# Performance work log

Hardware: AMD Instinct MI355X
Metric: run time of the kernel (lower is better)

Reference implementation:

```python
import jax, jax.numpy as jnp
import numpy as np

DIM = 33  # hardcoded in the torch module


def setup_inputs() -> dict:
    key = jax.random.key(0)
    k1, k2, k3 = jax.random.split(key, 3)
    B, H, W = 8, 512, 512
    inp = jax.random.uniform(k1, (B, 3, H, W), dtype=jnp.float32)
    out = jax.random.uniform(k2, (B, 3, H, W), dtype=jnp.float32)
    mask = (jax.random.uniform(k3, (B, 1, H, W)) > 0.5).astype(jnp.float32)
    return {"mask": mask, "input": inp, "output": out}


def _tridistribute(mask, inp, out, dim=DIM):
    # Trilinear scatter-accumulate of `out` pixel colors into a per-image
    # 3D LUT indexed by `inp` pixel colors, masked, then count-normalized.
    B = inp.shape[0]
    binsize = 1.000001 / (dim - 1)
    x = inp / binsize                              # [B,3,H,W]
    idx = jnp.floor(x).astype(jnp.int32)           # lower bin ids, in [0, dim-2]
    frac = x - jnp.floor(x)                        # trilinear fractions
    r_id, g_id, b_id = idx[:, 0], idx[:, 1], idx[:, 2]
    rd = frac[:, 0].reshape(B, -1)                 # [B,N], N = H*W
    gd = frac[:, 1].reshape(B, -1)
    bd = frac[:, 2].reshape(B, -1)
    base = (r_id + g_id * dim + b_id * dim * dim).reshape(B, -1)  # flat corner 000
    m = (mask[:, 0] > 0).astype(inp.dtype).reshape(B, -1)
    ws, offs = [], []
    for db in (0, 1):
        for dg in (0, 1):
            for dr in (0, 1):
                w = ((rd if dr else 1 - rd) * (gd if dg else 1 - gd) * (bd if db else 1 - bd))
                ws.append(w * m)
                offs.append(dr + dg * dim + db * dim * dim)
    w_all = jnp.stack(ws, 0)                                        # [8,B,N]
    idx_all = base[None] + jnp.asarray(offs, jnp.int32)[:, None, None]  # [8,B,N]
    idx_flat = idx_all.transpose(1, 0, 2).reshape(B, -1)            # [B,8N]
    w_flat = w_all.transpose(1, 0, 2).reshape(B, -1)                # [B,8N]
    out_f = out.reshape(B, 3, -1)                                   # [B,3,N]
    vals = (w_all[:, :, None, :] * out_f[None]).transpose(1, 2, 0, 3).reshape(B, 3, -1)  # [B,3,8N]
    nbins = dim ** 3
    # scatter-add per batch element (vmap over B, then over 3 channels)
    lut = jax.vmap(lambda i, v: jax.vmap(lambda vc: jnp.zeros(nbins, inp.dtype).at[i].add(vc))(v))(idx_flat, vals)  # [B,3,nbins]
    cnt1 = jax.vmap(lambda i, w: jnp.zeros(nbins, inp.dtype).at[i].add(w))(idx_flat, w_flat)  # [B,nbins]
    cnt = jnp.broadcast_to(cnt1[:, None, :], lut.shape)             # same count for all 3 channels
    denom = jnp.where(cnt > 0, cnt, 1.0)
    lut = jnp.where(cnt > 0, lut / denom, 0.0)                      # tridistribute.divide
    shape5 = (B, 3, dim, dim, dim)
    return lut.reshape(shape5), cnt.reshape(shape5)


def reference(mask, input, output):
    lut, lut_count = _tridistribute(mask, input, output)
    return lut, lut_count, output
```

## Files before the change

### kernel.cpp

```cpp
#include <hip/hip_runtime.h>
#include <hip/hip_fp16.h>

#define DIM   33
#define NB    (DIM * DIM * DIM)
#define BATCH 8
#define HW    (512 * 512)
#define SLICE (DIM * DIM)
#define NK1   32
#define CAP1  4416
#define W1    256
#define SPAN1 1024
#define SUB2  4
#define NKEY  1024
#define CAP2  192
#define MAXC2 1120

#define G1_OFF 0
#define G2_OFF 256
#define NCNT   (G2_OFF + BATCH * NKEY)
#define A1     8448
#define S1     (BATCH * NK1 * CAP1)
#define A2     (A1 + 3 * S1)
#define S2     (BATCH * NKEY * CAP2)
#define WS_WORDS (A2 + 3 * S2)

static __device__ __forceinline__ unsigned f2h(float x) {
    return (unsigned)__half_as_ushort(__float2half(x));
}
static __device__ __forceinline__ float h2f(unsigned u) {
    return __half2float(__ushort_as_half((unsigned short)(u & 0xffffu)));
}
static __device__ __forceinline__ unsigned pack2(float a, float b) {
    return f2h(a) | (f2h(b) << 16);
}

__global__ __launch_bounds__(256) void zero_counters(int* __restrict__ ws)
{
    int i = blockIdx.x * 256 + threadIdx.x;
    if (i < NCNT) ws[i] = 0;
}

__global__ __launch_bounds__(256) void sort1(const float* __restrict__ mask,
                                             const float* __restrict__ inp,
                                             const float* __restrict__ outp,
                                             int* __restrict__ ws,
                                             float* __restrict__ outcopy)
{
    __shared__ int hist[NK1], basev[NK1], startL[NK1];
    __shared__ unsigned       stX[SPAN1];
    __shared__ unsigned       stY[SPAN1];
    __shared__ unsigned       o01[SPAN1];
    __shared__ unsigned short o2h[SPAN1];
    __shared__ unsigned short rnk[SPAN1];
    __shared__ unsigned short sidx[SPAN1];

    const int bid = blockIdx.x;
    const int w   = bid & (W1 - 1);
    const int b   = bid >> 8;

    if (threadIdx.x < NK1) hist[threadIdx.x] = 0;
    __syncthreads();

    const float binsize = 1.000001f / 32.0f;
    const size_t off = (size_t)w * SPAN1;
    const float* mk  = mask + (size_t)b * HW + off;
    const float* inR = inp  + (size_t)b * 3 * HW + off;
    const float* inG = inR + HW;
    const float* inB = inR + 2 * HW;
    const float* oR  = outp + (size_t)b * 3 * HW + off;
    const float* oG  = oR + HW;
    const float* oB  = oR + 2 * HW;
    float* cR = outcopy + (size_t)b * 3 * HW + off;
    float* cG = cR + HW;
    float* cB = cR + 2 * HW;

    const int o = threadIdx.x * 4;

    {
        float4 mv = *(const float4*)(mk + o);
        float4 rv = *(const float4*)(inR + o);
        float4 gv = *(const float4*)(inG + o);
        float4 bv = *(const float4*)(inB + o);
        float4 a0 = *(const float4*)(oR + o);
        float4 a1 = *(const float4*)(oG + o);
        float4 a2 = *(const float4*)(oB + o);

        *(float4*)(cR + o) = a0;
        *(float4*)(cG + o) = a1;
        *(float4*)(cB + o) = a2;

        float mm[4] = {mv.x, mv.y, mv.z, mv.w};
        float rr[4] = {rv.x, rv.y, rv.z, rv.w};
        float gg[4] = {gv.x, gv.y, gv.z, gv.w};
        float bb[4] = {bv.x, bv.y, bv.z, bv.w};
        float q0[4] = {a0.x, a0.y, a0.z, a0.w};
        float q1[4] = {a1.x, a1.y, a1.z, a1.w};
        float q2[4] = {a2.x, a2.y, a2.z, a2.w};
        #pragma unroll
        for (int r = 0; r < 4; ++r) {
            o01[o + r] = pack2(q0[r], q1[r]);
            o2h[o + r] = (unsigned short)f2h(q2[r]);
            unsigned sx = 0, sy = 0;
            if (mm[r] > 0.0f) {
                float xr = rr[r] / binsize;
                float xg = gg[r] / binsize;
                float xb = bb[r] / binsize;
                float fr = floorf(xr), fg = floorf(xg), fb = floorf(xb);
                int ir = (int)fr, ig = (int)fg, ib = (int)fb;
                int rd12 = (int)((xr - fr) * 4095.0f + 0.5f);
                int gd12 = (int)((xg - fg) * 4095.0f + 0.5f);
                int bd12 = (int)((xb - fb) * 4095.0f + 0.5f);
                sx = (unsigned)ir | ((unsigned)ig << 5) | ((unsigned)rd12 << 10)
                   | ((unsigned)(gd12 & 0x3FF) << 22);
                sy = (unsigned)(gd12 >> 10) | ((unsigned)bd12 << 2)
                   | ((unsigned)ib << 14) | (1u << 19);
                rnk[o + r] = (unsigned short)atomicAdd(&hist[ib], 1);
            }
            stX[o + r] = sx;
            stY[o + r] = sy;
        }
    }
    __syncthreads();

    if (threadIdx.x < NK1) {
        int c = hist[threadIdx.x];
        basev[threadIdx.x] = c ? atomicAdd(&ws[G1_OFF + b * NK1 + threadIdx.x], c) : 0;
        int v = c;
        #pragma unroll
        for (int d = 1; d < 32; d <<= 1) {
            int t = __shfl_up(v, d);
            if (threadIdx.x >= d) v += t;
        }
        startL[threadIdx.x] = v - c;
    }
    __syncthreads();

    {
        #pragma unroll
        for (int r = 0; r < 4; ++r) {
            unsigned sy = stY[o + r];
            if (sy >> 19) {
                int k = (sy >> 14) & 31;
                sidx[startL[k] + rnk[o + r]] = (unsigned short)(o + r);
            }
        }
    }
    __syncthreads();

    const int nlive = startL[NK1 - 1] + hist[NK1 - 1];
    unsigned* x1 = (unsigned*)(ws + A1);
    unsigned* y1 = x1 + S1;
    unsigned* z1 = x1 + 2 * S1;
    for (int j = threadIdx.x; j < nlive; j += 256) {
        int t = sidx[j];
        unsigned sy = stY[t];
        int k = (sy >> 14) & 31;
        int gs = basev[k] + (j - startL[k]);
        if (gs < CAP1) {
            size_t base = (size_t)(b * NK1 + k) * CAP1 + gs;
            x1[base] = stX[t];
            y1[base] = (sy & 0x3FFFu) | ((o01[t] & 0xFFFFu) << 14);
            z1[base] = (o01[t] >> 16) | ((unsigned)o2h[t] << 16);
        }
    }
}

__global__ __launch_bounds__(256) void sort2(int* __restrict__ ws)
{
    __shared__ unsigned       xL[MAXC2], yL[MAXC2], zL[MAXC2];
    __shared__ unsigned short rnkL[MAXC2], sidxL[MAXC2];
    __shared__ int hist[32], basev[32], startL[32];

    const int bid = blockIdx.x;
    const int s   = bid & (SUB2 - 1);
    const int ib  = (bid >> 2) & 31;
    const int b   = bid >> 7;

    if (threadIdx.x < 32) hist[threadIdx.x] = 0;
    __syncthreads();

    int n1 = ws[G1_OFF + b * NK1 + ib];
    if (n1 > CAP1) n1 = CAP1;
    const int beg = n1 * s / SUB2;
    const int end = n1 * (s + 1) / SUB2;
    const int cntn = end - beg;

    const unsigned* x1 = (const unsigned*)(ws + A1);
    const unsigned* y1 = x1 + S1;
    const unsigned* z1 = x1 + 2 * S1;
    const size_t base1 = (size_t)(b * NK1 + ib) * CAP1 + beg;

    for (int i = threadIdx.x; i < cntn; i += 256) {
        unsigned x = x1[base1 + i];
        xL[i] = x;
        yL[i] = y1[base1 + i];
        zL[i] = z1[base1 + i];
        rnkL[i] = (unsigned short)atomicAdd(&hist[(x >> 5) & 31], 1);
    }
    __syncthreads();

    if (threadIdx.x < 32) {
        int c = hist[threadIdx.x];
        basev[threadIdx.x] = c
            ? atomicAdd(&ws[G2_OFF + ((b << 10) | (threadIdx.x << 5) | ib)], c) : 0;
        int v = c;
        #pragma unroll
        for (int d = 1; d < 32; d <<= 1) {
            int t = __shfl_up(v, d);
            if (threadIdx.x >= d) v += t;
        }
        startL[threadIdx.x] = v - c;
    }
    __syncthreads();

    for (int i = threadIdx.x; i < cntn; i += 256) {
        int k = (xL[i] >> 5) & 31;
        sidxL[startL[k] + rnkL[i]] = (unsigned short)i;
    }
    __syncthreads();

    unsigned* x2 = (unsigned*)(ws + A2);
    unsigned* y2 = x2 + S2;
    unsigned* z2 = x2 + 2 * S2;
    for (int j = threadIdx.x; j < cntn; j += 256) {
        int t = sidxL[j];
        unsigned x = xL[t];
        int k = (x >> 5) & 31;
        int gs = basev[k] + (j - startL[k]);
        if (gs < CAP2) {
            size_t b2 = (size_t)((b << 10) | (k << 5) | ib) * CAP2 + gs;
            x2[b2] = x;
            y2[b2] = yL[t];
            z2[b2] = zL[t];
        }
    }
}

__global__ __launch_bounds__(256) void gather_pass(const int* __restrict__ ws,
                                                   float* __restrict__ lut,
                                                   float* __restrict__ cnt)
{
    __shared__ float4         vK[4][2][CAP2];
    __shared__ unsigned short sidxL[4][CAP2];
    __shared__ int            histL[4][32];
    __shared__ int            startL[4][32];
    __shared__ float          partL[4][64][4];

    const int bid   = blockIdx.x;
    const int b     = bid / SLICE;
    const int rem   = bid % SLICE;
    const int gOut  = rem / DIM;
    const int blOut = rem % DIM;

    const int wv    = threadIdx.x >> 6;
    const int lane  = threadIdx.x & 63;
    const int ghalf = (wv >> 1) & 1;
    const int bhalf = wv & 1;
    const int ig    = gOut - 1 + ghalf;
    const int ib    = blOut - 1 + bhalf;
    const bool valid = ((unsigned)ig < 32u) && ((unsigned)ib < 32u);

    if (lane < 32) histL[wv][lane] = 0;
    __syncthreads();

    const unsigned* x2 = (const unsigned*)(ws + A2);
    const unsigned* y2 = x2 + S2;
    const unsigned* z2 = x2 + 2 * S2;

    const float inv = 1.0f / 4095.0f;
    int n = 0;
    int ranks[3] = {0, 0, 0};
    int irs[3]   = {0, 0, 0};
    if (valid) {
        int key = (ig << 5) | ib;
        n = ws[G2_OFF + ((b << 10) | key)];
        if (n > CAP2) n = CAP2;
        size_t kb = (size_t)((b << 10) | key) * CAP2;
        #pragma unroll
        for (int t = 0; t < 3; ++t) {
            int i = lane + t * 64;
            if (i < n) {
                unsigned x = x2[kb + i];
                unsigned y = y2[kb + i];
                unsigned z = z2[kb + i];
                float rd = (float)((x >> 10) & 0xFFF) * inv;
                float gd = (float)(((x >> 22) & 0x3FF) | ((y & 3u) << 10)) * inv;
                float bd = (float)((y >> 2) & 0xFFF) * inv;
                float o0 = h2f(y >> 14);
                float o1 = h2f(z);
                float o2 = h2f(z >> 16);
                float wg_ = ghalf ? (1.0f - gd) : gd;
                float wb_ = bhalf ? (1.0f - bd) : bd;
                float wgb = wg_ * wb_;
                float w0 = wgb * rd;
                float w1 = wgb * (1.0f - rd);
                vK[wv][0][i] = make_float4(w0 * o0, w0 * o1, w0 * o2, w0);
                vK[wv][1][i] = make_float4(w1 * o0, w1 * o1, w1 * o2, w1);
                irs[t] = x & 31;
                ranks[t] = atomicAdd(&histL[wv][irs[t]], 1);
            }
        }
    }
    __syncthreads();

    {
        int h = (lane < 32) ? histL[wv][lane] : 0;
        int v = h;
        #pragma unroll
        for (int o = 1; o < 32; o <<= 1) {
            int t = __shfl_up(v, o, 32);
            if ((lane & 31) >= o) v += t;
        }
        if (lane < 32) startL[wv][lane] = v - h;
    }
    __syncthreads();

    if (valid) {
        #pragma unroll
        for (int t = 0; t < 3; ++t) {
            int i = lane + t * 64;
            if (i < n)
                sidxL[wv][startL[wv][irs[t]] + ranks[t]] = (unsigned short)i;
        }
    }
    __syncthreads();

    float4 acc = make_float4(0.f, 0.f, 0.f, 0.f);
    if (valid) {
        const int run = lane >> 1;
        const int kk  = lane & 1;
        int s = startL[wv][run];
        int e = s + histL[wv][run];
        for (int j = s; j < e; ++j) {
            float4 v = vK[wv][kk][sidxL[wv][j]];
            acc.x += v.x; acc.y += v.y; acc.z += v.z; acc.w += v.w;
        }
    }
    *(float4*)partL[wv][lane] = acc;
    __syncthreads();

    if (threadIdx.x < DIM * 4) {
        int r  = threadIdx.x >> 2;
        int ch = threadIdx.x & 3;
        float v = 0.f, c = 0.f;
        #pragma unroll
        for (int w2 = 0; w2 < 4; ++w2) {
            if (r < 32) {
                v += partL[w2][2 * r + 1][ch == 3 ? 3 : ch];
                c += partL[w2][2 * r + 1][3];
            }
            if (r > 0) {
                v += partL[w2][2 * r - 2][ch == 3 ? 3 : ch];
                c += partL[w2][2 * r - 2][3];
            }
        }
        int bin = r + gOut * DIM + blOut * SLICE;
        size_t ob = (size_t)b * 3 * NB;
        if (ch == 3) {
            cnt[ob + bin]          = c;
            cnt[ob + NB + bin]     = c;
            cnt[ob + 2 * NB + bin] = c;
        } else {
            lut[ob + (size_t)ch * NB + bin] = (c > 0.0f) ? v / c : 0.0f;
        }
    }
}

__global__ void tridist_scatter(const float* __restrict__ mask,
                                const float* __restrict__ inp,
                                const float* __restrict__ outp,
                                float* __restrict__ lut,
                                float* __restrict__ cnt)
{
    int i = blockIdx.x * blockDim.x + threadIdx.x;
    if (i >= BATCH * HW) return;
    int b = i / HW;
    int p = i - b * HW;

    float m = mask[(size_t)b * HW + p];
    if (!(m > 0.0f)) return;

    const float binsize = 1.000001f / 32.0f;
    size_t ibase = (size_t)b * 3 * HW + p;
    float xr = inp[ibase] / binsize;
    float xg = inp[ibase + HW] / binsize;
    float xb = inp[ibase + 2 * HW] / binsize;
    float flr = floorf(xr), flg = floorf(xg), flb = floorf(xb);
    int ir = (int)flr, ig = (int)flg, ib = (int)flb;
    float rd = xr - flr, gd = xg - flg, bd = xb - flb;
    int base = ir + ig * DIM + ib * DIM * DIM;
    float o0 = outp[ibase], o1 = outp[ibase + HW], o2 = outp[ibase + 2 * HW];
    float wr[2] = {1.0f - rd, rd};
    float wg_[2] = {1.0f - gd, gd};
    float wb[2] = {1.0f - bd, bd};
    float* lut0 = lut + (size_t)b * 3 * NB;
    float* cnt0 = cnt + (size_t)b * 3 * NB;
    #pragma unroll
    for (int db = 0; db < 2; ++db)
        #pragma unroll
        for (int dg = 0; dg < 2; ++dg)
            #pragma unroll
            for (int dr = 0; dr < 2; ++dr) {
                float wv2 = (wr[dr] * wg_[dg]) * wb[db];
                int bin = base + dr + dg * DIM + db * DIM * DIM;
                atomicAdd(cnt0 + bin, wv2);
                atomicAdd(lut0 + bin, wv2 * o0);
                atomicAdd(lut0 + NB + bin, wv2 * o1);
                atomicAdd(lut0 + 2 * NB + bin, wv2 * o2);
            }
}

__global__ void tridist_finalize(float* __restrict__ lut, float* __restrict__ cnt)
{
    int i = blockIdx.x * blockDim.x + threadIdx.x;
    if (i >= BATCH * NB) return;
    int b = i / NB;
    int j = i - b * NB;
    float c = cnt[(size_t)b * 3 * NB + j];
    bool nz = (c > 0.0f);
    #pragma unroll
    for (int ch = 0; ch < 3; ++ch) {
        size_t off = ((size_t)b * 3 + ch) * NB + j;
        float v = lut[off];
        lut[off] = nz ? (v / c) : 0.0f;
        cnt[off] = c;
    }
}

__global__ void copy_out(const float4* __restrict__ src,
                         float4* __restrict__ dst, int n4)
{
    int i = blockIdx.x * blockDim.x + threadIdx.x;
    int stride = gridDim.x * blockDim.x;
    for (; i < n4; i += stride) dst[i] = src[i];
}

extern "C" void kernel_launch(void* const* d_in, const int* in_sizes, int n_in,
                              void* d_out, int out_size, void* d_ws, size_t ws_size,
                              hipStream_t stream)
{
    const float* mask = (const float*)d_in[0];
    const float* inp  = (const float*)d_in[1];
    const float* outp = (const float*)d_in[2];

    float* out     = (float*)d_out;
    float* lut     = out;
    float* cnt     = out + (size_t)BATCH * 3 * NB;
    float* outcopy = out + (size_t)2 * BATCH * 3 * NB;

    size_t need = (size_t)WS_WORDS * sizeof(int);

    if (ws_size >= need) {
        int* ws = (int*)d_ws;
        zero_counters<<<(NCNT + 255) / 256, 256, 0, stream>>>(ws);
        sort1<<<BATCH * W1, 256, 0, stream>>>(mask, inp, outp, ws, outcopy);
        sort2<<<BATCH * NK1 * SUB2, 256, 0, stream>>>(ws);
        gather_pass<<<BATCH * SLICE, 256, 0, stream>>>(ws, lut, cnt);
    } else {
        hipMemsetAsync(out, 0, (size_t)2 * BATCH * 3 * NB * sizeof(float), stream);
        tridist_scatter<<<(BATCH * HW + 255) / 256, 256, 0, stream>>>(mask, inp, outp, lut, cnt);
        tridist_finalize<<<(BATCH * NB + 255) / 256, 256, 0, stream>>>(lut, cnt);
        int n4 = BATCH * 3 * HW / 4;
        copy_out<<<2048, 256, 0, stream>>>((const float4*)outp, (float4*)outcopy, n4);
    }
}
```

Before: 71.65 us.

## Sort second pass fully by (g,r) bins and precompute run offsets for gather

The second sort pass now uses one 1024-thread block per (batch, b-bin) and sorts entries by the combined g and r bin in a single 1024-bin histogram and block-wide scan. It writes per-key counts and per-r run offsets into a new workspace table, so the global atomics and the counter zeroing for the second level go away. The gather kernel then reads contiguous runs directly instead of rebuilding a local histogram, scan and index permutation, which removes two barriers and the shared-memory indirection. In exchange, fewer and larger sort blocks run, and the data is read from global memory twice instead of being staged in LDS.

Result: slower. 78.74 us (+9.9%).

```diff
diff --git a/kernel.cpp b/kernel.cpp
--- a/kernel.cpp
+++ b/kernel.cpp
@@ -10,19 +10,19 @@
 #define CAP1  4416
 #define W1    256
 #define SPAN1 1024
-#define SUB2  4
 #define NKEY  1024
 #define CAP2  192
-#define MAXC2 1120
 
 #define G1_OFF 0
 #define G2_OFF 256
-#define NCNT   (G2_OFF + BATCH * NKEY)
+#define NCNT   256
 #define A1     8448
 #define S1     (BATCH * NK1 * CAP1)
 #define A2     (A1 + 3 * S1)
 #define S2     (BATCH * NKEY * CAP2)
-#define WS_WORDS (A2 + 3 * S2)
+#define RT_OFF (A2 + 3 * S2)
+#define RT_U16 (BATCH * NKEY * 32)
+#define WS_WORDS (RT_OFF + RT_U16 / 2)
 
 static __device__ __forceinline__ unsigned f2h(float x) {
     return (unsigned)__half_as_ushort(__float2half(x));
@@ -165,86 +165,109 @@
     }
 }
 
-__global__ __launch_bounds__(256) void sort2(int* __restrict__ ws)
-{
-    __shared__ unsigned       xL[MAXC2], yL[MAXC2], zL[MAXC2];
-    __shared__ unsigned short rnkL[MAXC2], sidxL[MAXC2];
-    __shared__ int hist[32], basev[32], startL[32];
-
-    const int bid = blockIdx.x;
-    const int s   = bid & (SUB2 - 1);
-    const int ib  = (bid >> 2) & 31;
-    const int b   = bid >> 7;
-
-    if (threadIdx.x < 32) hist[threadIdx.x] = 0;
+__global__ __launch_bounds__(1024) void sort2(int* __restrict__ ws,
+                                              unsigned short* __restrict__ runsT)
+{
+    __shared__ int hist[1024];
+    __shared__ int startL[1024];
+    __shared__ int wsum[16];
+
+    const int ib = blockIdx.x & 31;
+    const int b  = blockIdx.x >> 5;
+    const int tid = threadIdx.x;
+
+    hist[tid] = 0;
     __syncthreads();
 
     int n1 = ws[G1_OFF + b * NK1 + ib];
     if (n1 > CAP1) n1 = CAP1;
-    const int beg = n1 * s / SUB2;
-    const int end = n1 * (s + 1) / SUB2;
-    const int cntn = end - beg;
 
     const unsigned* x1 = (const unsigned*)(ws + A1);
     const unsigned* y1 = x1 + S1;
     const unsigned* z1 = x1 + 2 * S1;
-    const size_t base1 = (size_t)(b * NK1 + ib) * CAP1 + beg;
-
-    for (int i = threadIdx.x; i < cntn; i += 256) {
-        unsigned x = x1[base1 + i];
-        xL[i] = x;
-        yL[i] = y1[base1 + i];
-        zL[i] = z1[base1 + i];
-        rnkL[i] = (unsigned short)atomicAdd(&hist[(x >> 5) & 31], 1);
-    }
-    __syncthreads();
-
-    if (threadIdx.x < 32) {
-        int c = hist[threadIdx.x];
-        basev[threadIdx.x] = c
-            ? atomicAdd(&ws[G2_OFF + ((b << 10) | (threadIdx.x << 5) | ib)], c) : 0;
-        int v = c;
-        #pragma unroll
-        for (int d = 1; d < 32; d <<= 1) {
+    const size_t base1 = (size_t)(b * NK1 + ib) * CAP1;
+
+    int rnk[5], bins[5];
+    #pragma unroll
+    for (int k = 0; k < 5; ++k) {
+        int i = tid + k * 1024;
+        bins[k] = 0; rnk[k] = 0;
+        if (i < n1) {
+            unsigned x = x1[base1 + i];
+            int bin = (((x >> 5) & 31) << 5) | (x & 31);
+            bins[k] = bin;
+            rnk[k] = atomicAdd(&hist[bin], 1);
+        }
+    }
+    __syncthreads();
+
+    int h = hist[tid];
+    {
+        int lane = tid & 63, wid = tid >> 6;
+        int v = h;
+        #pragma unroll
+        for (int d = 1; d < 64; d <<= 1) {
             int t = __shfl_up(v, d);
-            if (threadIdx.x >= d) v += t;
-        }
-        startL[threadIdx.x] = v - c;
-    }
-    __syncthreads();
-
-    for (int i = threadIdx.x; i < cntn; i += 256) {
-        int k = (xL[i] >> 5) & 31;
-        sidxL[startL[k] + rnkL[i]] = (unsigned short)i;
-    }
-    __syncthreads();
+            if (lane >= d) v += t;
+        }
+        if (lane == 63) wsum[wid] = v;
+        __syncthreads();
+        if (tid < 16) {
+            int s = wsum[tid];
+            int v2 = s;
+            #pragma unroll
+            for (int d = 1; d < 16; d <<= 1) {
+                int t = __shfl_up(v2, d);
+                if (tid >= d) v2 += t;
+            }
+            wsum[tid] = v2 - s;
+        }
+        __syncthreads();
+        startL[tid] = v - h + wsum[wid];
+    }
+    __syncthreads();
+
+    {
+        int ig = tid >> 5, ir = tid & 31;
+        int key = (b << 10) | (ig << 5) | ib;
+        int keybase = startL[ig << 5];
+        if (ir == 0) {
+            int next = (ig == 31) ? n1 : startL[(ig + 1) << 5];
+            ws[G2_OFF + key] = next - keybase;
+            runsT[(size_t)key * 32] = 0;
+        } else {
+            runsT[(size_t)key * 32 + ir] =
+                (unsigned short)(startL[(ig << 5) | ir] - keybase);
+        }
+    }
 
     unsigned* x2 = (unsigned*)(ws + A2);
     unsigned* y2 = x2 + S2;
     unsigned* z2 = x2 + 2 * S2;
-    for (int j = threadIdx.x; j < cntn; j += 256) {
-        int t = sidxL[j];
-        unsigned x = xL[t];
-        int k = (x >> 5) & 31;
-        int gs = basev[k] + (j - startL[k]);
-        if (gs < CAP2) {
-            size_t b2 = (size_t)((b << 10) | (k << 5) | ib) * CAP2 + gs;
-            x2[b2] = x;
-            y2[b2] = yL[t];
-            z2[b2] = zL[t];
+    #pragma unroll
+    for (int k = 0; k < 5; ++k) {
+        int i = tid + k * 1024;
+        if (i < n1) {
+            int bin = bins[k];
+            int rel = startL[bin] - startL[bin & 0x3E0] + rnk[k];
+            if (rel < CAP2) {
+                int ig = bin >> 5;
+                size_t d = (size_t)((b << 10) | (ig << 5) | ib) * CAP2 + rel;
+                x2[d] = x1[base1 + i];
+                y2[d] = y1[base1 + i];
+                z2[d] = z1[base1 + i];
+            }
         }
     }
 }
 
 __global__ __launch_bounds__(256) void gather_pass(const int* __restrict__ ws,
+                                                   const unsigned short* __restrict__ runsT,
                                                    float* __restrict__ lut,
                                                    float* __restrict__ cnt)
 {
-    __shared__ float4         vK[4][2][CAP2];
-    __shared__ unsigned short sidxL[4][CAP2];
-    __shared__ int            histL[4][32];
-    __shared__ int            startL[4][32];
-    __shared__ float          partL[4][64][4];
+    __shared__ float4 vK[4][CAP2][2];
+    __shared__ float  partL[4][64][4];
 
     const int bid   = blockIdx.x;
     const int b     = bid / SLICE;
@@ -260,22 +283,26 @@
     const int ib    = blOut - 1 + bhalf;
     const bool valid = ((unsigned)ig < 32u) && ((unsigned)ib < 32u);
 
-    if (lane < 32) histL[wv][lane] = 0;
-    __syncthreads();
-
     const unsigned* x2 = (const unsigned*)(ws + A2);
     const unsigned* y2 = x2 + S2;
     const unsigned* z2 = x2 + 2 * S2;
 
     const float inv = 1.0f / 4095.0f;
-    int n = 0;
-    int ranks[3] = {0, 0, 0};
-    int irs[3]   = {0, 0, 0};
+    int myS = 0, myE = 0;
     if (valid) {
-        int key = (ig << 5) | ib;
-        n = ws[G2_OFF + ((b << 10) | key)];
+        int key = (b << 10) | (ig << 5) | ib;
+        int n = ws[G2_OFF + key];
         if (n > CAP2) n = CAP2;
-        size_t kb = (size_t)((b << 10) | key) * CAP2;
+
+        int tv = (lane < 32) ? (int)runsT[(size_t)key * 32 + lane] : 0;
+        int run = lane >> 1;
+        int s = __shfl(tv, run);
+        int e = (run == 31) ? n : __shfl(tv, run + 1);
+        if (s > n) s = n;
+        if (e > n) e = n;
+        myS = s; myE = e;
+
+        size_t kb = (size_t)key * CAP2;
         #pragma unroll
         for (int t = 0; t < 3; ++t) {
             int i = lane + t * 64;
@@ -294,45 +321,18 @@
                 float wgb = wg_ * wb_;
                 float w0 = wgb * rd;
                 float w1 = wgb * (1.0f - rd);
-                vK[wv][0][i] = make_float4(w0 * o0, w0 * o1, w0 * o2, w0);
-                vK[wv][1][i] = make_float4(w1 * o0, w1 * o1, w1 * o2, w1);
-                irs[t] = x & 31;
-                ranks[t] = atomicAdd(&histL[wv][irs[t]], 1);
-            }
-        }
-    }
-    __syncthreads();
-
-    {
-        int h = (lane < 32) ? histL[wv][lane] : 0;
-        int v = h;
-        #pragma unroll
-        for (int o = 1; o < 32; o <<= 1) {
-            int t = __shfl_up(v, o, 32);
-            if ((lane & 31) >= o) v += t;
-        }
-        if (lane < 32) startL[wv][lane] = v - h;
-    }
-    __syncthreads();
-
-    if (valid) {
-        #pragma unroll
-        for (int t = 0; t < 3; ++t) {
-            int i = lane + t * 64;
-            if (i < n)
-                sidxL[wv][startL[wv][irs[t]] + ranks[t]] = (unsigned short)i;
+                vK[wv][i][0] = make_float4(w0 * o0, w0 * o1, w0 * o2, w0);
+                vK[wv][i][1] = make_float4(w1 * o0, w1 * o1, w1 * o2, w1);
+            }
         }
     }
     __syncthreads();
 
     float4 acc = make_float4(0.f, 0.f, 0.f, 0.f);
     if (valid) {
-        const int run = lane >> 1;
-        const int kk  = lane & 1;
-        int s = startL[wv][run];
-        int e = s + histL[wv][run];
-        for (int j = s; j < e; ++j) {
-            float4 v = vK[wv][kk][sidxL[wv][j]];
+        const int kk = lane & 1;
+        for (int j = myS; j < myE; ++j) {
+            float4 v = vK[wv][j][kk];
             acc.x += v.x; acc.y += v.y; acc.z += v.z; acc.w += v.w;
         }
     }
@@ -452,10 +452,12 @@
 
     if (ws_size >= need) {
         int* ws = (int*)d_ws;
-        zero_counters<<<(NCNT + 255) / 256, 256, 0, stream>>>(ws);
+        unsigned short* runsT = (unsigned short*)((int*)d_ws + RT_OFF);
+
+        zero_counters<<<1, 256, 0, stream>>>(ws);
         sort1<<<BATCH * W1, 256, 0, stream>>>(mask, inp, outp, ws, outcopy);
-        sort2<<<BATCH * NK1 * SUB2, 256, 0, stream>>>(ws);
-        gather_pass<<<BATCH * SLICE, 256, 0, stream>>>(ws, lut, cnt);
+        sort2<<<BATCH * NK1, 1024, 0, stream>>>(ws, runsT);
+        gather_pass<<<BATCH * SLICE, 256, 0, stream>>>(ws, runsT, lut, cnt);
     } else {
         hipMemsetAsync(out, 0, (size_t)2 * BATCH * 3 * NB * sizeof(float), stream);
         tridist_scatter<<<(BATCH * HW + 255) / 256, 256, 0, stream>>>(mask, inp, outp, lut, cnt);
```
